# Kernel tuning notes

Hardware: AMD Instinct MI355X
Metric: run time of the kernel (lower is better)

Reference implementation:

```python
import jax, jax.numpy as jnp
import numpy as np

HEADS = 8
DIM_HEAD = 32
SCALE = DIM_HEAD ** -0.5


def _split_heads(t):
    # [b, n, h*d] -> [b, h, n, d]
    b, n, hd = t.shape
    return t.reshape(b, n, HEADS, hd // HEADS).transpose(0, 2, 1, 3)


def setup_inputs() -> dict:
    key = jax.random.key(0)
    k1, k2, k3, k4 = jax.random.split(key, 4)
    b, n, dim = 2, 2048, 256
    inner = HEADS * DIM_HEAD  # 256
    x = jax.random.normal(k1, (b, n, dim), dtype=jnp.float32)
    attn_feat = jax.random.normal(k2, (b, n, dim), dtype=jnp.float32)
    # nn.Linear(dim, 3*inner, bias=False): store as [dim, 3*inner] for x @ W
    W_qkv = jax.random.normal(k3, (dim, 3 * inner), dtype=jnp.float32) * (dim ** -0.5)
    W_qkv_aux = jax.random.normal(k4, (dim, 3 * inner), dtype=jnp.float32) * (dim ** -0.5)
    return {"x": x, "attn_feat": attn_feat, "W_qkv": W_qkv, "W_qkv_aux": W_qkv_aux,
            "use_cls_tokens": 1}


def reference(x, attn_feat, W_qkv, W_qkv_aux, use_cls_tokens):
    b, n, dim = x.shape
    # aux Q,K (v_aux computed but unused, matching original chunk of 3)
    qkv_aux = attn_feat @ W_qkv_aux            # [b, n, 3*inner]
    q_aux, k_aux, _ = jnp.split(qkv_aux, 3, axis=-1)
    q_aux, k_aux = _split_heads(q_aux), _split_heads(k_aux)
    # self Q,K
    qkv_self = x @ W_qkv
    q_self, k_self, _ = jnp.split(qkv_self, 3, axis=-1)
    q_self, k_self = _split_heads(q_self), _split_heads(k_self)
    # dual score product: (QK^T_aux * scale) * (QK^T_self * scale)
    dots_aux = jnp.einsum('bhid,bhjd->bhij', q_aux, k_aux) * SCALE
    dots_self = jnp.einsum('bhid,bhjd->bhij', q_self, k_self) * SCALE
    attn = jax.nn.softmax(dots_aux * dots_self, axis=-1)  # [b, h, n, n]
    # v = x.unsqueeze(1): broadcast raw x over heads
    out = jnp.einsum('bhij,bjd->bhid', attn, x)           # [b, h, n, dim]
    out = out.transpose(0, 2, 1, 3).reshape(b, n, HEADS * dim)
    attn_flat = attn.transpose(0, 2, 1, 3).reshape(b, n, HEADS * n)
    return (out, out[:, 0], attn_flat[:, 0])
```

## Files before the change

kernel.cpp:

```cpp
#include <hip/hip_runtime.h>

typedef _Float16 f16;
typedef _Float16 f16x4 __attribute__((ext_vector_type(4)));
typedef _Float16 f16x8 __attribute__((ext_vector_type(8)));
typedef float f32x4 __attribute__((ext_vector_type(4)));

#define LOG2E 1.4426950408889634f
#define SCL   (1.4426950408889634f / 32.0f)
#define TH_RAW 177.445f

__global__ __launch_bounds__(256) void k_transpose(const float* __restrict__ x,
                                                   f16* __restrict__ xt) {
  __shared__ f16 tile[64][65];
  int n0 = blockIdx.x * 64;
  int d0 = blockIdx.y * 64;
  int b  = blockIdx.z;
  int t = threadIdx.x;
  int colr = t & 63, rowg = t >> 6;
#pragma unroll
  for (int r = 0; r < 16; ++r) {
    int row = r * 4 + rowg;
    tile[row][colr] = (f16)x[((size_t)b * 2048 + n0 + row) * 256 + d0 + colr];
  }
  __syncthreads();
#pragma unroll
  for (int r = 0; r < 16; ++r) {
    int drow = r * 4 + rowg;
    xt[((size_t)b * 256 + d0 + drow) * 2048 + n0 + colr] = tile[colr][drow];
  }
}

__global__ __launch_bounds__(256) void k_transW(const float* __restrict__ Wq,
    const float* __restrict__ Wa, f16* __restrict__ Wt) {
  __shared__ f16 tile[64][65];
  int n0 = blockIdx.x * 64, k0 = blockIdx.y * 64, s = blockIdx.z;
  const float* W = s ? Wa : Wq;
  f16* dst = Wt + (size_t)s * 512 * 256;
  int t = threadIdx.x, c = t & 63, rg = t >> 6;
#pragma unroll
  for (int r = 0; r < 16; ++r) {
    int krow = r * 4 + rg;
    tile[krow][c] = (f16)W[(size_t)(k0 + krow) * 768 + n0 + c];
  }
  __syncthreads();
#pragma unroll
  for (int r = 0; r < 16; ++r) {
    int nrow = r * 4 + rg;
    dst[(size_t)(n0 + nrow) * 256 + k0 + c] = tile[c][nrow];
  }
}

__global__ __launch_bounds__(256) void k_proj(const float* __restrict__ x,
    const float* __restrict__ af, const f16* __restrict__ Wt,
    f16* __restrict__ Qs, f16* __restrict__ Ks,
    f16* __restrict__ Qa, f16* __restrict__ Ka) {
  int mt = blockIdx.x, nt = blockIdx.y, s = blockIdx.z;
  const float* A = s ? af : x;
  const f16* W = Wt + (size_t)s * 512 * 256;
  f16* Qd = s ? Qa : Qs;
  f16* Kd = s ? Ka : Ks;
  int t = threadIdx.x, wv = t >> 6, ln = t & 63, cl = ln & 15, g = ln >> 4;
  int m0 = mt * 64, n0 = nt * 64;
  const float* arow = A + (size_t)(m0 + wv * 16 + cl) * 256 + g * 8;
  const f16* wb = W + (size_t)n0 * 256 + g * 8;
  f32x4 z4 = {0.f, 0.f, 0.f, 0.f};
  f32x4 acc[4] = {z4, z4, z4, z4};
#pragma unroll
  for (int k32 = 0; k32 < 8; ++k32) {
    float4 u = *(const float4*)(arow + k32 * 32);
    float4 v = *(const float4*)(arow + k32 * 32 + 4);
    f16x8 a = { (f16)u.x, (f16)u.y, (f16)u.z, (f16)u.w,
                (f16)v.x, (f16)v.y, (f16)v.z, (f16)v.w };
#pragma unroll
    for (int n4 = 0; n4 < 4; ++n4) {
      f16x8 bf = *(const f16x8*)(wb + (size_t)(n4 * 16 + cl) * 256 + k32 * 32);
      acc[n4] = __builtin_amdgcn_mfma_f32_16x16x32_f16(a, bf, acc[n4], 0, 0, 0);
    }
  }
#pragma unroll
  for (int n4 = 0; n4 < 4; ++n4) {
    int c = n0 + n4 * 16 + cl;
    int head = (c & 255) >> 5, d = c & 31;
    f16* dst = (c < 256) ? Qd : Kd;
#pragma unroll
    for (int r = 0; r < 4; ++r) {
      int m = m0 + wv * 16 + g * 4 + r;
      int bb = m >> 11, nn = m & 2047;
      dst[(((size_t)bb * 8 + head) * 2048 + nn) * 32 + d] = (f16)acc[n4][r];
    }
  }
}

__global__ __launch_bounds__(256, 4) void k_flash(const f16* __restrict__ Qs,
    const f16* __restrict__ Ks, const f16* __restrict__ Qa,
    const f16* __restrict__ Ka, const f16* __restrict__ xt,
    float* __restrict__ out, float* __restrict__ out_cls) {
  __shared__ f16 KaL[2][64][40];
  __shared__ f16 KsL[2][64][40];
  __shared__ f16 PL[2][64][72];
  __shared__ float alphaL[2][64] __attribute__((aligned(16)));
  __shared__ int   rsF[2][4] __attribute__((aligned(16)));
  __shared__ float lL[64];
  int qt = blockIdx.x >> 1, ddh = blockIdx.x & 1;
  int h = blockIdx.y, b = blockIdx.z;
  int bh = b * 8 + h;
  int t = threadIdx.x, wv = t >> 6, ln = t & 63, cl = ln & 15, g = ln >> 4;
  int qrow0 = qt * 64 + wv * 16;
  f16x8 qsf = *(const f16x8*)&Qs[((size_t)bh * 2048 + qrow0 + cl) * 32 + g * 8];
  f16x8 qaf = *(const f16x8*)&Qa[((size_t)bh * 2048 + qrow0 + cl) * 32 + g * 8];
  f32x4 z4 = {0.f, 0.f, 0.f, 0.f};
  f32x4 acc[4][2];
#pragma unroll
  for (int i = 0; i < 4; ++i)
#pragma unroll
    for (int j = 0; j < 2; ++j) acc[i][j] = z4;
  float m_run = -3.0e38f, l_lane = 0.f;
  int krow = t >> 2, koff = (t & 3) * 8;
  const f16* kaSrc = Ka + ((size_t)bh * 2048 + krow) * 32 + koff;
  const f16* ksSrc = Ks + ((size_t)bh * 2048 + krow) * 32 + koff;
  const f16* xb = xt + ((size_t)b * 256 + ddh * 128 + wv * 32) * 2048;

  float tv[16];
  f16x8 xf[2][2];

  auto SCORE_MM = [&](int buf) {
#pragma unroll
    for (int jt = 0; jt < 4; ++jt) {
      f16x8 kaf = *(const f16x8*)&KaL[buf][jt * 16 + cl][g * 8];
      f16x8 ksf = *(const f16x8*)&KsL[buf][jt * 16 + cl][g * 8];
      f32x4 za = __builtin_amdgcn_mfma_f32_16x16x32_f16(kaf, qaf, z4, 0, 0, 0);
      f32x4 zs = __builtin_amdgcn_mfma_f32_16x16x32_f16(ksf, qsf, z4, 0, 0, 0);
#pragma unroll
      for (int r = 0; r < 4; ++r) tv[jt * 4 + r] = za[r] * zs[r];
    }
  };

  auto SCORE_FIN = [&](int buf) {
    float a0 = fmaxf(tv[0], tv[1]),   a1 = fmaxf(tv[2], tv[3]);
    float a2 = fmaxf(tv[4], tv[5]),   a3 = fmaxf(tv[6], tv[7]);
    float a4 = fmaxf(tv[8], tv[9]),   a5 = fmaxf(tv[10], tv[11]);
    float a6 = fmaxf(tv[12], tv[13]), a7 = fmaxf(tv[14], tv[15]);
    float b0 = fmaxf(a0, a1), b1 = fmaxf(a2, a3);
    float b2 = fmaxf(a4, a5), b3 = fmaxf(a6, a7);
    float lmax = fmaxf(fmaxf(b0, b1), fmaxf(b2, b3));
    int wflag = 0;
    if (__any(lmax > m_run + TH_RAW)) {
      float tm = fmaxf(lmax, __shfl_xor(lmax, 16, 64));
      tm = fmaxf(tm, __shfl_xor(tm, 32, 64));
      float m_new = fmaxf(m_run, tm);
      float alpha = exp2f((m_run - m_new) * SCL);
      l_lane *= alpha;
      m_run = m_new;
      if (g == 0) alphaL[buf][wv * 16 + cl] = alpha;
      wflag = 1;
    }
    float mS = m_run * SCL;
    float p[16];
#pragma unroll
    for (int i = 0; i < 16; ++i) p[i] = exp2f(fmaf(tv[i], SCL, -mS));
    float s0 = p[0] + p[1],   s1 = p[2] + p[3];
    float s2 = p[4] + p[5],   s3 = p[6] + p[7];
    float s4 = p[8] + p[9],   s5 = p[10] + p[11];
    float s6 = p[12] + p[13], s7 = p[14] + p[15];
    float u0 = s0 + s1, u1 = s2 + s3, u2 = s4 + s5, u3 = s6 + s7;
    l_lane += (u0 + u1) + (u2 + u3);
#pragma unroll
    for (int jt = 0; jt < 4; ++jt) {
      auto lo = __builtin_amdgcn_cvt_pkrtz(p[jt * 4 + 0], p[jt * 4 + 1]);
      auto hi = __builtin_amdgcn_cvt_pkrtz(p[jt * 4 + 2], p[jt * 4 + 3]);
      f16x4 pk = { (f16)lo[0], (f16)lo[1], (f16)hi[0], (f16)hi[1] };
      *(f16x4*)&PL[buf][wv * 16 + cl][jt * 16 + g * 4] = pk;
    }
    if (ln == 0) rsF[buf][wv] = wflag;
  };

  auto XFLOAD = [&](int kt) {
#pragma unroll
    for (int ks2 = 0; ks2 < 2; ++ks2)
#pragma unroll
      for (int ddt = 0; ddt < 2; ++ddt)
        xf[ks2][ddt] = *(const f16x8*)(xb + (size_t)(ddt * 16 + cl) * 2048 +
                                       kt * 64 + ks2 * 32 + g * 8);
  };

  auto PVDO = [&](int pbuf) {
    int4 fl = *(const int4*)&rsF[pbuf][0];
    int flq[4] = { fl.x, fl.y, fl.z, fl.w };
#pragma unroll
    for (int qt2 = 0; qt2 < 4; ++qt2) {
      if (flq[qt2]) {
        f32x4 a4 = *(const f32x4*)&alphaL[pbuf][qt2 * 16 + g * 4];
#pragma unroll
        for (int ddt = 0; ddt < 2; ++ddt)
#pragma unroll
          for (int r = 0; r < 4; ++r) acc[qt2][ddt][r] *= a4[r];
      }
    }
#pragma unroll
    for (int ks2 = 0; ks2 < 2; ++ks2) {
      f16x8 pf[4];
#pragma unroll
      for (int qt2 = 0; qt2 < 4; ++qt2)
        pf[qt2] = *(const f16x8*)&PL[pbuf][qt2 * 16 + cl][ks2 * 32 + g * 8];
#pragma unroll
      for (int ddt = 0; ddt < 2; ++ddt)
#pragma unroll
        for (int qt2 = 0; qt2 < 4; ++qt2)
          acc[qt2][ddt] = __builtin_amdgcn_mfma_f32_16x16x32_f16(
              pf[qt2], xf[ks2][ddt], acc[qt2][ddt], 0, 0, 0);
    }
  };

  *(f16x8*)&KaL[0][krow][koff] = *(const f16x8*)kaSrc;
  *(f16x8*)&KsL[0][krow][koff] = *(const f16x8*)ksSrc;
  __syncthreads();

  f16x8 kan = *(const f16x8*)(kaSrc + 2048);
  f16x8 ksn = *(const f16x8*)(ksSrc + 2048);
  SCORE_MM(0);
  SCORE_FIN(0);
  *(f16x8*)&KaL[1][krow][koff] = kan;
  *(f16x8*)&KsL[1][krow][koff] = ksn;
  __syncthreads();

  for (int k = 1; k < 32; ++k) {
    int sbuf = k & 1, pbuf = sbuf ^ 1;
    XFLOAD(k - 1);
    if (k < 31) {
      kan = *(const f16x8*)(kaSrc + (size_t)(k + 1) * 2048);
      ksn = *(const f16x8*)(ksSrc + (size_t)(k + 1) * 2048);
    }
    SCORE_MM(sbuf);
    PVDO(pbuf);
    SCORE_FIN(sbuf);
    if (k < 31) {
      *(f16x8*)&KaL[pbuf][krow][koff] = kan;
      *(f16x8*)&KsL[pbuf][krow][koff] = ksn;
    }
    __syncthreads();
  }

  XFLOAD(31);
  PVDO(1);

  l_lane += __shfl_xor(l_lane, 16, 64);
  l_lane += __shfl_xor(l_lane, 32, 64);
  if (g == 0) lL[wv * 16 + cl] = l_lane;
  __syncthreads();
#pragma unroll
  for (int qt2 = 0; qt2 < 4; ++qt2) {
#pragma unroll
    for (int r = 0; r < 4; ++r) {
      float linv = 1.0f / lL[qt2 * 16 + g * 4 + r];
      int q = qt * 64 + qt2 * 16 + g * 4 + r;
#pragma unroll
      for (int ddt = 0; ddt < 2; ++ddt) {
        float v = acc[qt2][ddt][r] * linv;
        int col = h * 256 + ddh * 128 + wv * 32 + ddt * 16 + cl;
        out[((size_t)b * 2048 + q) * 2048 + col] = v;
        if (q == 0) out_cls[(size_t)b * 2048 + col] = v;
      }
    }
  }
}

__global__ __launch_bounds__(256) void k_attn0(const f16* __restrict__ Qs,
    const f16* __restrict__ Ks, const f16* __restrict__ Qa,
    const f16* __restrict__ Ka, float* __restrict__ dst) {
  __shared__ float qa_s[32], qs_s[32];
  __shared__ float red[256];
  int h = blockIdx.x, b = blockIdx.y, bh = b * 8 + h;
  int t = threadIdx.x;
  if (t < 32) {
    qa_s[t] = (float)Qa[(size_t)bh * 2048 * 32 + t];
    qs_s[t] = (float)Qs[(size_t)bh * 2048 * 32 + t];
  }
  __syncthreads();
  float sv[8];
#pragma unroll
  for (int r = 0; r < 8; ++r) {
    int j = r * 256 + t;
    const f16x8* ka8 = (const f16x8*)&Ka[((size_t)bh * 2048 + j) * 32];
    const f16x8* ks8 = (const f16x8*)&Ks[((size_t)bh * 2048 + j) * 32];
    float da = 0.f, ds = 0.f;
#pragma unroll
    for (int c = 0; c < 4; ++c) {
      f16x8 va = ka8[c], vs = ks8[c];
#pragma unroll
      for (int d = 0; d < 8; ++d) {
        da += qa_s[c * 8 + d] * (float)va[d];
        ds += qs_s[c * 8 + d] * (float)vs[d];
      }
    }
    sv[r] = da * ds * (1.f / 32.f);
  }
  float mx = sv[0];
#pragma unroll
  for (int r = 1; r < 8; ++r) mx = fmaxf(mx, sv[r]);
  red[t] = mx;
  __syncthreads();
  for (int st = 128; st > 0; st >>= 1) {
    if (t < st) red[t] = fmaxf(red[t], red[t + st]);
    __syncthreads();
  }
  float m = red[0];
  __syncthreads();
  float e[8], sum = 0.f;
#pragma unroll
  for (int r = 0; r < 8; ++r) {
    e[r] = exp2f((sv[r] - m) * LOG2E);
    sum += e[r];
  }
  red[t] = sum;
  __syncthreads();
  for (int st = 128; st > 0; st >>= 1) {
    if (t < st) red[t] += red[t + st];
    __syncthreads();
  }
  float l = red[0];
#pragma unroll
  for (int r = 0; r < 8; ++r)
    dst[(size_t)b * 16384 + h * 2048 + r * 256 + t] = e[r] / l;
}

extern "C" void kernel_launch(void* const* d_in, const int* in_sizes, int n_in,
                              void* d_out, int out_size, void* d_ws, size_t ws_size,
                              hipStream_t stream) {
  const float* x  = (const float*)d_in[0];
  const float* af = (const float*)d_in[1];
  const float* Wq = (const float*)d_in[2];
  const float* Wa = (const float*)d_in[3];
  const size_t QK = (size_t)2 * 8 * 2048 * 32;
  f16* Qs = (f16*)d_ws;
  f16* Ks = Qs + QK;
  f16* Qa = Ks + QK;
  f16* Ka = Qa + QK;
  f16* xt = Ka + QK;
  f16* Wt = xt + QK;
  float* out     = (float*)d_out;
  float* out_cls = out + (size_t)2 * 2048 * 2048;
  float* attn0   = out_cls + 2 * 2048;

  k_transpose<<<dim3(32, 4, 2), 256, 0, stream>>>(x, xt);
  k_transW<<<dim3(8, 4, 2), 256, 0, stream>>>(Wq, Wa, Wt);
  k_proj<<<dim3(64, 8, 2), 256, 0, stream>>>(x, af, Wt, Qs, Ks, Qa, Ka);
  k_flash<<<dim3(64, 8, 2), 256, 0, stream>>>(Qs, Ks, Qa, Ka, xt, out, out_cls);
  k_attn0<<<dim3(8, 2), 256, 0, stream>>>(Qs, Ks, Qa, Ka, attn0);
}
```

Before: 194.7 us.

## Widen flash tiles to full head dim, fuse attn0 and transpose kernels

Each flash block now covers all 256 output columns of x instead of splitting them into two 128-column halves. The score computation (QK products, softmax) is therefore done once per query tile rather than twice. Block 0 of each (b,h) row computes the first-row attention probabilities inside the flash launch, and the two transpose kernels are merged into one launch, cutting the launch count from five to three. The cost is twice the accumulator registers with occupancy hint lowered from 4 to 2 blocks, and half as many flash blocks, which may lower parallelism on a large GPU.

After: 175.3 us. 10.0% less time.

```diff
diff --git a/kernel.cpp b/kernel.cpp
--- a/kernel.cpp
+++ b/kernel.cpp
@@ -9,44 +9,39 @@
 #define SCL   (1.4426950408889634f / 32.0f)
 #define TH_RAW 177.445f
 
-__global__ __launch_bounds__(256) void k_transpose(const float* __restrict__ x,
-                                                   f16* __restrict__ xt) {
+__global__ __launch_bounds__(256) void k_stage(const float* __restrict__ x,
+    const float* __restrict__ Wq, const float* __restrict__ Wa,
+    f16* __restrict__ xt, f16* __restrict__ Wt) {
   __shared__ f16 tile[64][65];
-  int n0 = blockIdx.x * 64;
-  int d0 = blockIdx.y * 64;
-  int b  = blockIdx.z;
-  int t = threadIdx.x;
-  int colr = t & 63, rowg = t >> 6;
-#pragma unroll
-  for (int r = 0; r < 16; ++r) {
-    int row = r * 4 + rowg;
-    tile[row][colr] = (f16)x[((size_t)b * 2048 + n0 + row) * 256 + d0 + colr];
-  }
-  __syncthreads();
-#pragma unroll
-  for (int r = 0; r < 16; ++r) {
-    int drow = r * 4 + rowg;
-    xt[((size_t)b * 256 + d0 + drow) * 2048 + n0 + colr] = tile[colr][drow];
-  }
-}
-
-__global__ __launch_bounds__(256) void k_transW(const float* __restrict__ Wq,
-    const float* __restrict__ Wa, f16* __restrict__ Wt) {
-  __shared__ f16 tile[64][65];
-  int n0 = blockIdx.x * 64, k0 = blockIdx.y * 64, s = blockIdx.z;
-  const float* W = s ? Wa : Wq;
-  f16* dst = Wt + (size_t)s * 512 * 256;
   int t = threadIdx.x, c = t & 63, rg = t >> 6;
-#pragma unroll
-  for (int r = 0; r < 16; ++r) {
-    int krow = r * 4 + rg;
-    tile[krow][c] = (f16)W[(size_t)(k0 + krow) * 768 + n0 + c];
-  }
-  __syncthreads();
-#pragma unroll
-  for (int r = 0; r < 16; ++r) {
-    int nrow = r * 4 + rg;
-    dst[(size_t)(n0 + nrow) * 256 + k0 + c] = tile[c][nrow];
+  if (blockIdx.x < 32) {
+    int n0 = blockIdx.x * 64, d0 = blockIdx.y * 64, b = blockIdx.z;
+#pragma unroll
+    for (int r = 0; r < 16; ++r) {
+      int row = r * 4 + rg;
+      tile[row][c] = (f16)x[((size_t)b * 2048 + n0 + row) * 256 + d0 + c];
+    }
+    __syncthreads();
+#pragma unroll
+    for (int r = 0; r < 16; ++r) {
+      int drow = r * 4 + rg;
+      xt[((size_t)b * 256 + d0 + drow) * 2048 + n0 + c] = tile[c][drow];
+    }
+  } else {
+    int n0 = (blockIdx.x - 32) * 64, k0 = blockIdx.y * 64, s = blockIdx.z;
+    const float* W = s ? Wa : Wq;
+    f16* dst = Wt + (size_t)s * 512 * 256;
+#pragma unroll
+    for (int r = 0; r < 16; ++r) {
+      int krow = r * 4 + rg;
+      tile[krow][c] = (f16)W[(size_t)(k0 + krow) * 768 + n0 + c];
+    }
+    __syncthreads();
+#pragma unroll
+    for (int r = 0; r < 16; ++r) {
+      int nrow = r * 4 + rg;
+      dst[(size_t)(n0 + nrow) * 256 + k0 + c] = tile[c][nrow];
+    }
   }
 }
 
@@ -91,37 +86,97 @@
   }
 }
 
-__global__ __launch_bounds__(256, 4) void k_flash(const f16* __restrict__ Qs,
+__global__ __launch_bounds__(256, 2) void k_flash(const f16* __restrict__ Qs,
     const f16* __restrict__ Ks, const f16* __restrict__ Qa,
     const f16* __restrict__ Ka, const f16* __restrict__ xt,
-    float* __restrict__ out, float* __restrict__ out_cls) {
+    float* __restrict__ out, float* __restrict__ out_cls,
+    float* __restrict__ attn0) {
   __shared__ f16 KaL[2][64][40];
   __shared__ f16 KsL[2][64][40];
   __shared__ f16 PL[2][64][72];
   __shared__ float alphaL[2][64] __attribute__((aligned(16)));
   __shared__ int   rsF[2][4] __attribute__((aligned(16)));
   __shared__ float lL[64];
-  int qt = blockIdx.x >> 1, ddh = blockIdx.x & 1;
   int h = blockIdx.y, b = blockIdx.z;
   int bh = b * 8 + h;
-  int t = threadIdx.x, wv = t >> 6, ln = t & 63, cl = ln & 15, g = ln >> 4;
+  int t = threadIdx.x;
+
+  if (blockIdx.x == 0) {
+    float* qa_s = &alphaL[0][0];
+    float* qs_s = &alphaL[1][0];
+    float* red  = (float*)&PL[0][0][0];
+    if (t < 32) {
+      qa_s[t] = (float)Qa[(size_t)bh * 2048 * 32 + t];
+      qs_s[t] = (float)Qs[(size_t)bh * 2048 * 32 + t];
+    }
+    __syncthreads();
+    float sv[8];
+#pragma unroll
+    for (int r = 0; r < 8; ++r) {
+      int j = r * 256 + t;
+      const f16x8* ka8 = (const f16x8*)&Ka[((size_t)bh * 2048 + j) * 32];
+      const f16x8* ks8 = (const f16x8*)&Ks[((size_t)bh * 2048 + j) * 32];
+      float da = 0.f, ds = 0.f;
+#pragma unroll
+      for (int c = 0; c < 4; ++c) {
+        f16x8 va = ka8[c], vs = ks8[c];
+#pragma unroll
+        for (int d = 0; d < 8; ++d) {
+          da += qa_s[c * 8 + d] * (float)va[d];
+          ds += qs_s[c * 8 + d] * (float)vs[d];
+        }
+      }
+      sv[r] = da * ds * (1.f / 32.f);
+    }
+    float mx = sv[0];
+#pragma unroll
+    for (int r = 1; r < 8; ++r) mx = fmaxf(mx, sv[r]);
+    red[t] = mx;
+    __syncthreads();
+    for (int st = 128; st > 0; st >>= 1) {
+      if (t < st) red[t] = fmaxf(red[t], red[t + st]);
+      __syncthreads();
+    }
+    float m = red[0];
+    __syncthreads();
+    float e[8], sum = 0.f;
+#pragma unroll
+    for (int r = 0; r < 8; ++r) {
+      e[r] = exp2f((sv[r] - m) * LOG2E);
+      sum += e[r];
+    }
+    red[t] = sum;
+    __syncthreads();
+    for (int st = 128; st > 0; st >>= 1) {
+      if (t < st) red[t] += red[t + st];
+      __syncthreads();
+    }
+    float l = red[0];
+#pragma unroll
+    for (int r = 0; r < 8; ++r)
+      attn0[(size_t)b * 16384 + h * 2048 + r * 256 + t] = e[r] / l;
+    return;
+  }
+
+  int qt = blockIdx.x - 1;
+  int wv = t >> 6, ln = t & 63, cl = ln & 15, g = ln >> 4;
   int qrow0 = qt * 64 + wv * 16;
   f16x8 qsf = *(const f16x8*)&Qs[((size_t)bh * 2048 + qrow0 + cl) * 32 + g * 8];
   f16x8 qaf = *(const f16x8*)&Qa[((size_t)bh * 2048 + qrow0 + cl) * 32 + g * 8];
   f32x4 z4 = {0.f, 0.f, 0.f, 0.f};
-  f32x4 acc[4][2];
+  f32x4 acc[4][4];
 #pragma unroll
   for (int i = 0; i < 4; ++i)
 #pragma unroll
-    for (int j = 0; j < 2; ++j) acc[i][j] = z4;
+    for (int j = 0; j < 4; ++j) acc[i][j] = z4;
   float m_run = -3.0e38f, l_lane = 0.f;
   int krow = t >> 2, koff = (t & 3) * 8;
   const f16* kaSrc = Ka + ((size_t)bh * 2048 + krow) * 32 + koff;
   const f16* ksSrc = Ks + ((size_t)bh * 2048 + krow) * 32 + koff;
-  const f16* xb = xt + ((size_t)b * 256 + ddh * 128 + wv * 32) * 2048;
+  const f16* xb = xt + ((size_t)b * 256 + wv * 64) * 2048;
 
   float tv[16];
-  f16x8 xf[2][2];
+  f16x8 xf[2][4];
 
   auto SCORE_MM = [&](int buf) {
 #pragma unroll
@@ -178,7 +233,7 @@
 #pragma unroll
     for (int ks2 = 0; ks2 < 2; ++ks2)
 #pragma unroll
-      for (int ddt = 0; ddt < 2; ++ddt)
+      for (int ddt = 0; ddt < 4; ++ddt)
         xf[ks2][ddt] = *(const f16x8*)(xb + (size_t)(ddt * 16 + cl) * 2048 +
                                        kt * 64 + ks2 * 32 + g * 8);
   };
@@ -191,7 +246,7 @@
       if (flq[qt2]) {
         f32x4 a4 = *(const f32x4*)&alphaL[pbuf][qt2 * 16 + g * 4];
 #pragma unroll
-        for (int ddt = 0; ddt < 2; ++ddt)
+        for (int ddt = 0; ddt < 4; ++ddt)
 #pragma unroll
           for (int r = 0; r < 4; ++r) acc[qt2][ddt][r] *= a4[r];
       }
@@ -203,7 +258,7 @@
       for (int qt2 = 0; qt2 < 4; ++qt2)
         pf[qt2] = *(const f16x8*)&PL[pbuf][qt2 * 16 + cl][ks2 * 32 + g * 8];
 #pragma unroll
-      for (int ddt = 0; ddt < 2; ++ddt)
+      for (int ddt = 0; ddt < 4; ++ddt)
 #pragma unroll
         for (int qt2 = 0; qt2 < 4; ++qt2)
           acc[qt2][ddt] = __builtin_amdgcn_mfma_f32_16x16x32_f16(
@@ -254,73 +309,14 @@
       float linv = 1.0f / lL[qt2 * 16 + g * 4 + r];
       int q = qt * 64 + qt2 * 16 + g * 4 + r;
 #pragma unroll
-      for (int ddt = 0; ddt < 2; ++ddt) {
+      for (int ddt = 0; ddt < 4; ++ddt) {
         float v = acc[qt2][ddt][r] * linv;
-        int col = h * 256 + ddh * 128 + wv * 32 + ddt * 16 + cl;
+        int col = h * 256 + wv * 64 + ddt * 16 + cl;
         out[((size_t)b * 2048 + q) * 2048 + col] = v;
         if (q == 0) out_cls[(size_t)b * 2048 + col] = v;
       }
     }
   }
-}
-
-__global__ __launch_bounds__(256) void k_attn0(const f16* __restrict__ Qs,
-    const f16* __restrict__ Ks, const f16* __restrict__ Qa,
-    const f16* __restrict__ Ka, float* __restrict__ dst) {
-  __shared__ float qa_s[32], qs_s[32];
-  __shared__ float red[256];
-  int h = blockIdx.x, b = blockIdx.y, bh = b * 8 + h;
-  int t = threadIdx.x;
-  if (t < 32) {
-    qa_s[t] = (float)Qa[(size_t)bh * 2048 * 32 + t];
-    qs_s[t] = (float)Qs[(size_t)bh * 2048 * 32 + t];
-  }
-  __syncthreads();
-  float sv[8];
-#pragma unroll
-  for (int r = 0; r < 8; ++r) {
-    int j = r * 256 + t;
-    const f16x8* ka8 = (const f16x8*)&Ka[((size_t)bh * 2048 + j) * 32];
-    const f16x8* ks8 = (const f16x8*)&Ks[((size_t)bh * 2048 + j) * 32];
-    float da = 0.f, ds = 0.f;
-#pragma unroll
-    for (int c = 0; c < 4; ++c) {
-      f16x8 va = ka8[c], vs = ks8[c];
-#pragma unroll
-      for (int d = 0; d < 8; ++d) {
-        da += qa_s[c * 8 + d] * (float)va[d];
-        ds += qs_s[c * 8 + d] * (float)vs[d];
-      }
-    }
-    sv[r] = da * ds * (1.f / 32.f);
-  }
-  float mx = sv[0];
-#pragma unroll
-  for (int r = 1; r < 8; ++r) mx = fmaxf(mx, sv[r]);
-  red[t] = mx;
-  __syncthreads();
-  for (int st = 128; st > 0; st >>= 1) {
-    if (t < st) red[t] = fmaxf(red[t], red[t + st]);
-    __syncthreads();
-  }
-  float m = red[0];
-  __syncthreads();
-  float e[8], sum = 0.f;
-#pragma unroll
-  for (int r = 0; r < 8; ++r) {
-    e[r] = exp2f((sv[r] - m) * LOG2E);
-    sum += e[r];
-  }
-  red[t] = sum;
-  __syncthreads();
-  for (int st = 128; st > 0; st >>= 1) {
-    if (t < st) red[t] += red[t + st];
-    __syncthreads();
-  }
-  float l = red[0];
-#pragma unroll
-  for (int r = 0; r < 8; ++r)
-    dst[(size_t)b * 16384 + h * 2048 + r * 256 + t] = e[r] / l;
 }
 
 extern "C" void kernel_launch(void* const* d_in, const int* in_sizes, int n_in,
@@ -341,9 +337,8 @@
   float* out_cls = out + (size_t)2 * 2048 * 2048;
   float* attn0   = out_cls + 2 * 2048;
 
-  k_transpose<<<dim3(32, 4, 2), 256, 0, stream>>>(x, xt);
-  k_transW<<<dim3(8, 4, 2), 256, 0, stream>>>(Wq, Wa, Wt);
+  k_stage<<<dim3(40, 4, 2), 256, 0, stream>>>(x, Wq, Wa, xt, Wt);
   k_proj<<<dim3(64, 8, 2), 256, 0, stream>>>(x, af, Wt, Qs, Ks, Qa, Ka);
-  k_flash<<<dim3(64, 8, 2), 256, 0, stream>>>(Qs, Ks, Qa, Ka, xt, out, out_cls);
-  k_attn0<<<dim3(8, 2), 256, 0, stream>>>(Qs, Ks, Qa, Ka, attn0);
+  k_flash<<<dim3(33, 8, 2), 256, 0, stream>>>(Qs, Ks, Qa, Ka, xt, out, out_cls,
+                                              attn0);
 }
```
